# Kernel optimization log

Measured on AMD Instinct MI355X. Metric: run time of the kernel, lower is better.

## Reference

```python
import jax, jax.numpy as jnp
import numpy as np

# Graph layout: B equal-sized graphs, contiguous node ids.
B, NG, EG = 64, 2000, 64000          # graphs, nodes/graph, edges/graph
K = 1600                              # ceil(0.8 * NG) — TopKPooling ratio=0.8
N, E = B * NG, B * EG
FEAT_DIM, EMB, G1, G2, DENSE, NCLS = 10000, 64, 32, 32, 64, 10


def setup_inputs() -> dict:
    key = jax.random.key(0)
    ks = jax.random.split(key, 12)
    x = jax.random.randint(ks[0], (N, 1), 0, FEAT_DIM)
    # random edges within each graph, then offset by graph base node id
    e = jax.random.randint(ks[1], (2, B, EG), 0, NG) + (jnp.arange(B) * NG)[None, :, None]
    edge_index = e.reshape(2, E)
    batch = jnp.repeat(jnp.arange(B), NG)
    sc = 0.05
    return {
        "x": x, "edge_index": edge_index, "batch": batch,
        "emb": jax.random.normal(ks[2], (FEAT_DIM, EMB), jnp.float32) * sc,
        "W1": jax.random.normal(ks[3], (EMB, G1), jnp.float32) * sc,
        "b1": jnp.zeros((G1,), jnp.float32),
        "W2": jax.random.normal(ks[4], (G1, G2), jnp.float32) * sc,
        "b2": jnp.zeros((G2,), jnp.float32),
        "pool_w": jax.random.normal(ks[5], (G2,), jnp.float32) * sc,
        "dense_W": jax.random.normal(ks[6], (G2, DENSE), jnp.float32) * sc,
        "dense_b": jnp.zeros((DENSE,), jnp.float32),
        "out_W": jax.random.normal(ks[7], (DENSE, NCLS), jnp.float32) * sc,
        "out_b": jnp.zeros((NCLS,), jnp.float32),
    }


def gcn_layer(h, src, dst, W, b):
    """PyG GCNConv: add self-loops, symmetric D^-1/2 A D^-1/2 aggregation."""
    n = h.shape[0]
    loop = jnp.arange(n)
    s = jnp.concatenate([src, loop])
    d = jnp.concatenate([dst, loop])
    h = h @ W                                                   # [N, out]
    deg = jax.ops.segment_sum(jnp.ones_like(d, dtype=h.dtype), d, num_segments=n)
    dinv = jnp.where(deg > 0, deg ** -0.5, 0.0)
    norm = dinv[s] * dinv[d]                                    # [E+N]
    out = jax.ops.segment_sum(h[s] * norm[:, None], d, num_segments=n)
    return out + b


def reference(x, edge_index, batch, emb, W1, b1, W2, b2, pool_w,
              dense_W, dense_b, out_W, out_b):
    h = emb[x[:, 0]]                                            # [N, EMB]
    src, dst = edge_index[0], edge_index[1]
    h = jax.nn.relu(gcn_layer(h, src, dst, W1, b1))
    h = jax.nn.relu(gcn_layer(h, src, dst, W2, b2))
    # TopKPooling: score = tanh(x.w / ||w||); keep top ceil(0.8*NG) per graph,
    # scale kept features by their scores. Equal graph sizes -> static shapes.
    score = jnp.tanh(h @ pool_w / jnp.linalg.norm(pool_w))      # [N]
    sb = score.reshape(B, NG)
    hb = h.reshape(B, NG, G2)
    vals, idx = jax.lax.top_k(sb, K)                            # [B, K]
    hp = jnp.take_along_axis(hb, idx[:, :, None], axis=1) * vals[:, :, None]
    g = hp.max(axis=1)                                          # global max pool [B, G2]
    d = jax.nn.relu(g @ dense_W + dense_b)
    return d @ out_W + out_b                                    # [B, NCLS]
```

## Files before the change

### kernel.cpp

```cpp
#include <hip/hip_runtime.h>
#include <hip/hip_fp16.h>
#include <math.h>

#define NB 64
#define NGRAPH 2000
#define EGRAPH 64000
#define NN (NB*NGRAPH)
#define NE (NB*EGRAPH)
#define KSEL 1600
#define FEAT 10000
#define EMBD 64
#define G1D 32
#define G2D 32
#define DENSED 64
#define NCLSD 10
#define NCHUNK 8
#define CHUNK_E (EGRAPH/NCHUNK)
#define NQD 8
#define QNODES (NGRAPH/NQD)
#define LOUT_CAP 10000


__device__ __forceinline__ float4 ld_row8h(const char* base, unsigned byteoff)
{
    uint2 u = *(const uint2*)(base + byteoff);
    __half2 p0 = *(__half2*)&u.x;
    __half2 p1 = *(__half2*)&u.y;
    float2 f0 = __half22float2(p0);
    float2 f1 = __half22float2(p1);
    return make_float4(f0.x, f0.y, f1.x, f1.y);
}

__device__ __forceinline__ void st_row8h(__half* dst, float4 v)
{
    __half2 p0 = __floats2half2_rn(v.x, v.y);
    __half2 p1 = __floats2half2_rn(v.z, v.w);
    uint2 u;
    u.x = *(unsigned*)&p0;
    u.y = *(unsigned*)&p1;
    *(uint2*)dst = u;
}

__global__ __launch_bounds__(256) void prep_kernel(const int* __restrict__ ei,
                                                   int* __restrict__ chist,
                                                   const float* __restrict__ emb,
                                                   const float* __restrict__ W1,
                                                   float* __restrict__ embW)
{
    __shared__ float shmem[2048];
    const int tid = threadIdx.x;
    if (blockIdx.x < 512) {
        int* hist = (int*)shmem;
        const int lb = blockIdx.x;
        const int xcd = lb & 7, t = lb >> 3;
        const int g = xcd * 8 + (t >> 3);
        const int q = t & 7;
        const int base_e = g * EGRAPH + q * CHUNK_E;
        const int base_n = g * NGRAPH;
        for (int v = tid; v < NGRAPH; v += 256) hist[v] = 0;
        __syncthreads();
        for (int k = tid; k < CHUNK_E; k += 256) {
            int d = ei[NE + base_e + k];
            atomicAdd(&hist[d - base_n], 1);
        }
        __syncthreads();
        int* out = chist + (size_t)(g * NCHUNK + q) * NGRAPH;
        for (int v = tid; v < NGRAPH; v += 256) out[v] = hist[v];
    } else {
        float* W1s = shmem;
        for (int i = tid; i < EMBD * G1D; i += 256) W1s[i] = W1[i];
        __syncthreads();
        int id = (blockIdx.x - 512) * 256 + tid;
        int r = id >> 5, c = id & 31;
        if (r >= FEAT) return;
        const float* er = emb + r * EMBD;
        float acc = 0.f;
        #pragma unroll 8
        for (int k = 0; k < EMBD; ++k) acc += er[k] * W1s[k * G1D + c];
        embW[r * G1D + c] = acc;
    }
}

__global__ __launch_bounds__(256) void scan_graph(const int* __restrict__ chist,
                                                  float* __restrict__ dinv,
                                                  int* __restrict__ row_start)
{
    __shared__ int hist[NGRAPH];
    __shared__ int csA[256];
    __shared__ int csB[256];
    const int b = (blockIdx.x & 7) * 8 + (blockIdx.x >> 3);
    const int tid = threadIdx.x;
    const int base_n = b * NGRAPH, base_e = b * EGRAPH;
    const int* ch = chist + (size_t)b * NCHUNK * NGRAPH;

    for (int v = tid; v < NGRAPH; v += 256) {
        int tot = 0;
        #pragma unroll
        for (int q = 0; q < NCHUNK; ++q) tot += ch[q * NGRAPH + v];
        hist[v] = tot;
        dinv[base_n + v] = rsqrtf((float)(tot + 1));
    }
    __syncthreads();
    if (tid < 250) {
        int s = 0;
        #pragma unroll
        for (int i = 0; i < 8; ++i) s += hist[tid * 8 + i];
        csA[tid] = s;
    }
    __syncthreads();
    int* sb = csA; int* db = csB;
    for (int off = 1; off < 256; off <<= 1) {
        int v = 0;
        if (tid < 250) { v = sb[tid]; if (tid >= off) v += sb[tid - off]; }
        if (tid < 250) db[tid] = v;
        __syncthreads();
        int* t = sb; sb = db; db = t;
    }
    if (tid < 250) {
        int run = (tid == 0) ? 0 : sb[tid - 1];
        #pragma unroll
        for (int i = 0; i < 8; ++i) {
            int idx = tid * 8 + i;
            int c = hist[idx];
            row_start[base_n + idx] = base_e + run;
            run += c;
        }
    }
}

__global__ __launch_bounds__(1024) void mid_kernel(const int* __restrict__ ei,
                                                   const int* __restrict__ row_start,
                                                   int* __restrict__ csr,
                                                   const int* __restrict__ x,
                                                   const float* __restrict__ embW,
                                                   const float* __restrict__ dinv,
                                                   __half* __restrict__ A)
{
    __shared__ int cur[QNODES];
    __shared__ int lout[LOUT_CAP];
    const int tid = threadIdx.x;
    if (blockIdx.x < 512) {
        const int lb = blockIdx.x;
        const int xcd = lb & 7, t = lb >> 3;
        const int g = xcd * 8 + (t >> 3);
        const int qd = t & 7;
        const int base_n = g * NGRAPH;
        const int lo = qd * QNODES;
        const int base = row_start[base_n + lo];
        const int qend = (g == NB - 1 && qd == NQD - 1) ? NE
                         : row_start[base_n + lo + QNODES];
        for (int v = tid; v < QNODES; v += 1024)
            cur[v] = row_start[base_n + lo + v] - base;
        __syncthreads();
        const int4* srcp = (const int4*)(ei + g * EGRAPH);
        const int4* dstp = (const int4*)(ei + NE + g * EGRAPH);
        const int sub = base_n + lo;
        for (int k = tid; k < EGRAPH / 4; k += 1024) {
            int4 d4 = dstp[k];
            int4 s4 = srcp[k];
            int d, pos;
            d = d4.x - sub;
            if ((unsigned)d < (unsigned)QNODES) {
                pos = atomicAdd(&cur[d], 1);
                if (pos < LOUT_CAP) lout[pos] = s4.x << 6;
            }
            d = d4.y - sub;
            if ((unsigned)d < (unsigned)QNODES) {
                pos = atomicAdd(&cur[d], 1);
                if (pos < LOUT_CAP) lout[pos] = s4.y << 6;
            }
            d = d4.z - sub;
            if ((unsigned)d < (unsigned)QNODES) {
                pos = atomicAdd(&cur[d], 1);
                if (pos < LOUT_CAP) lout[pos] = s4.z << 6;
            }
            d = d4.w - sub;
            if ((unsigned)d < (unsigned)QNODES) {
                pos = atomicAdd(&cur[d], 1);
                if (pos < LOUT_CAP) lout[pos] = s4.w << 6;
            }
        }
        __syncthreads();
        int size = qend - base;
        if (size > LOUT_CAP) size = LOUT_CAP;
        for (int i = tid; i < size; i += 1024)
            csr[base + i] = lout[i];
    } else {
        int id = (blockIdx.x - 512) * 1024 + tid;
        int v = id >> 3, r = id & 7;
        int xv = x[v];
        float dv = dinv[v];
        float4 e = ((const float4*)(embW + (size_t)xv * G1D))[r];
        e.x *= dv; e.y *= dv; e.z *= dv; e.w *= dv;
        st_row8h(A + (size_t)v * G1D + r * 4, e);
    }
}


__global__ __launch_bounds__(256) void agg1_kernel(const __half* __restrict__ Ain,
                                                   const float* __restrict__ dinv,
                                                   const int* __restrict__ row_start,
                                                   const int* __restrict__ csr,
                                                   const float* __restrict__ b1,
                                                   const float* __restrict__ W2,
                                                   __half* __restrict__ Bout)
{
    __shared__ float hsh[8][G2D];
    const int lb = blockIdx.x;
    const int xcd = lb & 7, idx = lb >> 3;
    const int b = xcd * 8 + (idx >> 5);
    const int blk = idx & 31;
    const int half_id = threadIdx.x >> 5;
    const int hl = threadIdx.x & 31;
    const int slot = hl >> 3;
    const int r = hl & 7;
    const int roff = r << 3;
    const char* Abase = (const char*)Ain;
    const int base_n = b * NGRAPH;
    const float4 bias4 = ((const float4*)b1)[r];

    float w2c[G1D];
    #pragma unroll
    for (int k = 0; k < G1D; ++k) w2c[k] = W2[k * G2D + hl];

    const int vloc0 = blk * 64 + half_id * 8;
    int v = base_n + ((vloc0 < NGRAPH) ? vloc0 : NGRAPH - 1);
    int rs = row_start[v];
    int re = (v == NN - 1) ? NE : row_start[v + 1];
    int s0 = csr[rs + slot];
    int s1 = csr[rs + slot + 4];
    int s2 = csr[rs + slot + 8];
    int s3 = csr[rs + slot + 12];

    for (int i = 0; i < 8; ++i) {
        int vloc = vloc0 + i;
        if (vloc >= NGRAPH) break;
        int re_next = (v + 1 >= NN - 1) ? NE : row_start[v + 2];
        int n0 = csr[re + slot];
        int n1 = csr[re + slot + 4];
        int n2 = csr[re + slot + 8];
        int n3 = csr[re + slot + 12];

        int me = rs + ((re - rs) & ~15);
        float4 acc0 = make_float4(0.f, 0.f, 0.f, 0.f);
        float4 acc1 = make_float4(0.f, 0.f, 0.f, 0.f);
        float4 acc2 = make_float4(0.f, 0.f, 0.f, 0.f);
        float4 acc3 = make_float4(0.f, 0.f, 0.f, 0.f);
        if (slot == 0)
            acc0 = ld_row8h(Abase, (unsigned)(v * (G1D * 2) + roff));
        int j = rs + slot;
        while (j < me) {
            int jn = j + 16;
            int t0 = csr[jn];
            int t1 = csr[jn + 4];
            int t2 = csr[jn + 8];
            int t3 = csr[jn + 12];
            float4 a0 = ld_row8h(Abase, (unsigned)(s0 + roff));
            float4 a1 = ld_row8h(Abase, (unsigned)(s1 + roff));
            float4 a2 = ld_row8h(Abase, (unsigned)(s2 + roff));
            float4 a3 = ld_row8h(Abase, (unsigned)(s3 + roff));
            acc0.x += a0.x; acc0.y += a0.y; acc0.z += a0.z; acc0.w += a0.w;
            acc1.x += a1.x; acc1.y += a1.y; acc1.z += a1.z; acc1.w += a1.w;
            acc2.x += a2.x; acc2.y += a2.y; acc2.z += a2.z; acc2.w += a2.w;
            acc3.x += a3.x; acc3.y += a3.y; acc3.z += a3.z; acc3.w += a3.w;
            j = jn; s0 = t0; s1 = t1; s2 = t2; s3 = t3;
        }
        {
            int jt = me + slot;
            if (jt < re) {
                float4 a = ld_row8h(Abase, (unsigned)(s0 + roff));
                acc0.x += a.x; acc0.y += a.y; acc0.z += a.z; acc0.w += a.w;
            }
            if (jt + 4 < re) {
                float4 a = ld_row8h(Abase, (unsigned)(s1 + roff));
                acc1.x += a.x; acc1.y += a.y; acc1.z += a.z; acc1.w += a.w;
            }
            if (jt + 8 < re) {
                float4 a = ld_row8h(Abase, (unsigned)(s2 + roff));
                acc2.x += a.x; acc2.y += a.y; acc2.z += a.z; acc2.w += a.w;
            }
            if (jt + 12 < re) {
                float4 a = ld_row8h(Abase, (unsigned)(s3 + roff));
                acc3.x += a.x; acc3.y += a.y; acc3.z += a.z; acc3.w += a.w;
            }
        }
        float4 acc;
        acc.x = (acc0.x + acc1.x) + (acc2.x + acc3.x);
        acc.y = (acc0.y + acc1.y) + (acc2.y + acc3.y);
        acc.z = (acc0.z + acc1.z) + (acc2.z + acc3.z);
        acc.w = (acc0.w + acc1.w) + (acc2.w + acc3.w);
        #pragma unroll
        for (int off = 8; off <= 16; off <<= 1) {
            acc.x += __shfl_xor(acc.x, off, 32);
            acc.y += __shfl_xor(acc.y, off, 32);
            acc.z += __shfl_xor(acc.z, off, 32);
            acc.w += __shfl_xor(acc.w, off, 32);
        }
        float dv = dinv[v];
        if (slot == 0) {
            float4 h4;
            h4.x = fmaxf(dv * acc.x + bias4.x, 0.f);
            h4.y = fmaxf(dv * acc.y + bias4.y, 0.f);
            h4.z = fmaxf(dv * acc.z + bias4.z, 0.f);
            h4.w = fmaxf(dv * acc.w + bias4.w, 0.f);
            ((float4*)&hsh[half_id][0])[r] = h4;
        }
        float o0 = 0.f, o1 = 0.f, o2 = 0.f, o3 = 0.f;
        const float4* hrow = (const float4*)&hsh[half_id][0];
        #pragma unroll
        for (int q = 0; q < 8; ++q) {
            float4 hh = hrow[q];
            o0 += hh.x * w2c[4 * q + 0];
            o1 += hh.y * w2c[4 * q + 1];
            o2 += hh.z * w2c[4 * q + 2];
            o3 += hh.w * w2c[4 * q + 3];
        }
        Bout[(size_t)v * G2D + hl] = __float2half(dv * ((o0 + o1) + (o2 + o3)));
        v = v + 1;
        rs = re; re = re_next; s0 = n0; s1 = n1; s2 = n2; s3 = n3;
    }
}

__global__ __launch_bounds__(256) void agg2_kernel(const __half* __restrict__ Bin,
                                                   const float* __restrict__ dinv,
                                                   const int* __restrict__ row_start,
                                                   const int* __restrict__ csr,
                                                   const float* __restrict__ b2,
                                                   const float* __restrict__ pool_w,
                                                   __half* __restrict__ h2out,
                                                   float* __restrict__ scores)
{
    const int lb = blockIdx.x;
    const int xcd = lb & 7, idx = lb >> 3;
    const int b = xcd * 8 + (idx >> 5);
    const int blk = idx & 31;
    const int half_id = threadIdx.x >> 5;
    const int hl = threadIdx.x & 31;
    const int slot = hl >> 3;
    const int r = hl & 7;
    const int roff = r << 3;
    const char* Bbase = (const char*)Bin;
    const int base_n = b * NGRAPH;
    const float4 bias4 = ((const float4*)b2)[r];
    const float4 pw4 = ((const float4*)pool_w)[r];

    float pw = pool_w[hl];
    float nsq = pw * pw;
    #pragma unroll
    for (int off = 16; off; off >>= 1) nsq += __shfl_xor(nsq, off, 32);
    const float inv_norm = rsqrtf(nsq);

    const int vloc0 = blk * 64 + half_id * 8;
    int v = base_n + ((vloc0 < NGRAPH) ? vloc0 : NGRAPH - 1);
    int rs = row_start[v];
    int re = (v == NN - 1) ? NE : row_start[v + 1];
    int s0 = csr[rs + slot];
    int s1 = csr[rs + slot + 4];
    int s2 = csr[rs + slot + 8];
    int s3 = csr[rs + slot + 12];

    for (int i = 0; i < 8; ++i) {
        int vloc = vloc0 + i;
        if (vloc >= NGRAPH) break;
        int re_next = (v + 1 >= NN - 1) ? NE : row_start[v + 2];
        int n0 = csr[re + slot];
        int n1 = csr[re + slot + 4];
        int n2 = csr[re + slot + 8];
        int n3 = csr[re + slot + 12];

        int me = rs + ((re - rs) & ~15);
        float4 acc0 = make_float4(0.f, 0.f, 0.f, 0.f);
        float4 acc1 = make_float4(0.f, 0.f, 0.f, 0.f);
        float4 acc2 = make_float4(0.f, 0.f, 0.f, 0.f);
        float4 acc3 = make_float4(0.f, 0.f, 0.f, 0.f);
        if (slot == 0)
            acc0 = ld_row8h(Bbase, (unsigned)(v * (G2D * 2) + roff));
        int j = rs + slot;
        while (j < me) {
            int jn = j + 16;
            int t0 = csr[jn];
            int t1 = csr[jn + 4];
            int t2 = csr[jn + 8];
            int t3 = csr[jn + 12];
            float4 a0 = ld_row8h(Bbase, (unsigned)(s0 + roff));
            float4 a1 = ld_row8h(Bbase, (unsigned)(s1 + roff));
            float4 a2 = ld_row8h(Bbase, (unsigned)(s2 + roff));
            float4 a3 = ld_row8h(Bbase, (unsigned)(s3 + roff));
            acc0.x += a0.x; acc0.y += a0.y; acc0.z += a0.z; acc0.w += a0.w;
            acc1.x += a1.x; acc1.y += a1.y; acc1.z += a1.z; acc1.w += a1.w;
            acc2.x += a2.x; acc2.y += a2.y; acc2.z += a2.z; acc2.w += a2.w;
            acc3.x += a3.x; acc3.y += a3.y; acc3.z += a3.z; acc3.w += a3.w;
            j = jn; s0 = t0; s1 = t1; s2 = t2; s3 = t3;
        }
        {
            int jt = me + slot;
            if (jt < re) {
                float4 a = ld_row8h(Bbase, (unsigned)(s0 + roff));
                acc0.x += a.x; acc0.y += a.y; acc0.z += a.z; acc0.w += a.w;
            }
            if (jt + 4 < re) {
                float4 a = ld_row8h(Bbase, (unsigned)(s1 + roff));
                acc1.x += a.x; acc1.y += a.y; acc1.z += a.z; acc1.w += a.w;
            }
            if (jt + 8 < re) {
                float4 a = ld_row8h(Bbase, (unsigned)(s2 + roff));
                acc2.x += a.x; acc2.y += a.y; acc2.z += a.z; acc2.w += a.w;
            }
            if (jt + 12 < re) {
                float4 a = ld_row8h(Bbase, (unsigned)(s3 + roff));
                acc3.x += a.x; acc3.y += a.y; acc3.z += a.z; acc3.w += a.w;
            }
        }
        float4 acc;
        acc.x = (acc0.x + acc1.x) + (acc2.x + acc3.x);
        acc.y = (acc0.y + acc1.y) + (acc2.y + acc3.y);
        acc.z = (acc0.z + acc1.z) + (acc2.z + acc3.z);
        acc.w = (acc0.w + acc1.w) + (acc2.w + acc3.w);
        #pragma unroll
        for (int off = 8; off <= 16; off <<= 1) {
            acc.x += __shfl_xor(acc.x, off, 32);
            acc.y += __shfl_xor(acc.y, off, 32);
            acc.z += __shfl_xor(acc.z, off, 32);
            acc.w += __shfl_xor(acc.w, off, 32);
        }
        float dv = dinv[v];
        float4 h4;
        h4.x = fmaxf(dv * acc.x + bias4.x, 0.f);
        h4.y = fmaxf(dv * acc.y + bias4.y, 0.f);
        h4.z = fmaxf(dv * acc.z + bias4.z, 0.f);
        h4.w = fmaxf(dv * acc.w + bias4.w, 0.f);
        if (slot == 0)
            st_row8h(h2out + (size_t)v * G2D + r * 4, h4);
        float t = h4.x * pw4.x + h4.y * pw4.y + h4.z * pw4.z + h4.w * pw4.w;
        t += __shfl_xor(t, 1, 32);
        t += __shfl_xor(t, 2, 32);
        t += __shfl_xor(t, 4, 32);
        if (hl == 0) scores[v] = tanhf(t * inv_norm);
        v = v + 1;
        rs = re; re = re_next; s0 = n0; s1 = n1; s2 = n2; s3 = n3;
    }
}

__global__ __launch_bounds__(256) void topk_pool_mlp(const __half* __restrict__ h2,
                                                     const float* __restrict__ scores,
                                                     const float* __restrict__ dense_W,
                                                     const float* __restrict__ dense_b,
                                                     const float* __restrict__ out_W,
                                                     const float* __restrict__ out_b,
                                                     float* __restrict__ out)
{
    __shared__ unsigned keys[NGRAPH];
    __shared__ float    sval[NGRAPH];
    __shared__ unsigned char inc[NGRAPH];
    __shared__ int  hist[256];
    __shared__ int  csA[256];
    __shared__ int  csB[256];
    __shared__ int  sel[2];
    __shared__ int  redc[4];
    __shared__ float redf[32][32];
    __shared__ float gvec[32];
    __shared__ float dvec[DENSED];
    const int b = (blockIdx.x & 7) * 8 + (blockIdx.x >> 3);
    const int tid = threadIdx.x;
    const int base_n = b * NGRAPH;

    for (int v = tid; v < NGRAPH; v += 256) {
        float f = scores[base_n + v];
        sval[v] = f;
        unsigned u = __float_as_uint(f);
        keys[v] = (u & 0x80000000u) ? ~u : (u | 0x80000000u);
    }
    __syncthreads();

    unsigned T = 0;
    int need = KSEL;
    #pragma unroll
    for (int pass = 0; pass < 4; ++pass) {
        const int s = 24 - pass * 8;
        const unsigned hi_mask = (pass == 0) ? 0u : (0xFFFFFFFFu << (s + 8));
        hist[tid] = 0;
        __syncthreads();
        for (int v = tid; v < NGRAPH; v += 256) {
            unsigned k = keys[v];
            if ((k & hi_mask) == (T & hi_mask))
                atomicAdd(&hist[(k >> s) & 255], 1);
        }
        __syncthreads();
        csA[tid] = hist[255 - tid];
        __syncthreads();
        int* sb = csA; int* db = csB;
        for (int off = 1; off < 256; off <<= 1) {
            int val = sb[tid];
            if (tid >= off) val += sb[tid - off];
            db[tid] = val;
            __syncthreads();
            int* t = sb; sb = db; db = t;
        }
        {
            const int d = tid;
            int suf_d = sb[255 - d];
            int suf_d1 = (d == 255) ? 0 : sb[254 - d];
            if (suf_d >= need && suf_d1 < need) {
                sel[0] = d;
                sel[1] = suf_d1;
            }
        }
        __syncthreads();
        T |= ((unsigned)sel[0]) << s;
        need -= sel[1];
        __syncthreads();
    }

    const int wid = tid >> 6, ln = tid & 63;
    int cg = 0, ce = 0;
    for (int v = tid; v < NGRAPH; v += 256) {
        cg += (keys[v] > T) ? 1 : 0;
        ce += (keys[v] == T) ? 1 : 0;
    }
    int packed = (cg << 16) | ce;
    #pragma unroll
    for (int off = 32; off; off >>= 1) packed += __shfl_down(packed, off, 64);
    if (ln == 0) redc[wid] = packed;
    __syncthreads();
    int tot = redc[0] + redc[1] + redc[2] + redc[3];
    int m_gt = tot >> 16, m_eq = tot & 0xffff;
    int needed = KSEL - m_gt;
    float fT = (T & 0x80000000u) ? __uint_as_float(T & 0x7fffffffu)
                                 : __uint_as_float(~T);
    if (m_eq == needed || fT == 0.0f) {
        for (int v = tid; v < NGRAPH; v += 256) inc[v] = (keys[v] >= T) ? 1 : 0;
    } else {
        if (tid == 0) {
            int take = 0;
            for (int v = 0; v < NGRAPH; ++v) {
                unsigned k = keys[v];
                if (k > T) inc[v] = 1;
                else if (k == T && take < needed) { inc[v] = 1; ++take; }
                else inc[v] = 0;
            }
        }
    }
    __syncthreads();

    {
        const int rowslot = tid >> 3;
        const int c4 = tid & 7;
        float4 m4 = make_float4(-INFINITY, -INFINITY, -INFINITY, -INFINITY);
        const char* h2base = (const char*)h2;
        for (int v = rowslot; v < NGRAPH; v += 32) {
            float4 hrow = ld_row8h(h2base,
                                   (unsigned)((base_n + v) * (G2D * 2) + c4 * 8));
            float sv = inc[v] ? sval[v] : 0.f;
            float big = inc[v] ? 0.f : -INFINITY;
            m4.x = fmaxf(m4.x, sv * hrow.x + big);
            m4.y = fmaxf(m4.y, sv * hrow.y + big);
            m4.z = fmaxf(m4.z, sv * hrow.z + big);
            m4.w = fmaxf(m4.w, sv * hrow.w + big);
        }
        redf[rowslot][c4 * 4 + 0] = m4.x;
        redf[rowslot][c4 * 4 + 1] = m4.y;
        redf[rowslot][c4 * 4 + 2] = m4.z;
        redf[rowslot][c4 * 4 + 3] = m4.w;
    }
    __syncthreads();
    if (tid < 32) {
        float g = redf[0][tid];
        #pragma unroll
        for (int rr = 1; rr < 32; ++rr) g = fmaxf(g, redf[rr][tid]);
        gvec[tid] = g;
    }
    __syncthreads();
    if (tid < DENSED) {
        float t = dense_b[tid];
        #pragma unroll
        for (int k = 0; k < G2D; ++k) t += gvec[k] * dense_W[k * DENSED + tid];
        dvec[tid] = fmaxf(t, 0.f);
    }
    __syncthreads();
    if (tid < NCLSD) {
        float o = out_b[tid];
        #pragma unroll
        for (int j = 0; j < DENSED; ++j) o += dvec[j] * out_W[j * NCLSD + tid];
        out[b * NCLSD + tid] = o;
    }
}

extern "C" void kernel_launch(void* const* d_in, const int* in_sizes, int n_in,
                              void* d_out, int out_size, void* d_ws, size_t ws_size,
                              hipStream_t stream)
{
    (void)in_sizes; (void)n_in; (void)out_size; (void)ws_size;
    const int*   x       = (const int*)  d_in[0];
    const int*   edge    = (const int*)  d_in[1];
    const float* emb     = (const float*)d_in[3];
    const float* W1      = (const float*)d_in[4];
    const float* b1      = (const float*)d_in[5];
    const float* W2      = (const float*)d_in[6];
    const float* b2      = (const float*)d_in[7];
    const float* pool_w  = (const float*)d_in[8];
    const float* dense_W = (const float*)d_in[9];
    const float* dense_b = (const float*)d_in[10];
    const float* out_W   = (const float*)d_in[11];
    const float* out_b   = (const float*)d_in[12];
    float* outp = (float*)d_out;

    char* ws = (char*)d_ws;
    float*  embW      = (float*)ws;
    __half* Ah        = (__half*)(ws + 1280000);
    __half* Bh        = (__half*)(ws + 1280000 + 8192000);
    float*  dinv      = (float*)(ws + 1280000 + 2*8192000);
    int*    row_start = (int*)((char*)dinv + (size_t)NN*4);
    int*    csr       = (int*)((char*)row_start + (size_t)NN*4);
    float*  scores    = (float*)((char*)csr + (size_t)(NE+16)*4);

    int* chist = (int*)Bh;

    prep_kernel<<<512 + (FEAT * G1D) / 256, 256, 0, stream>>>(edge, chist, emb, W1, embW);
    scan_graph<<<NB, 256, 0, stream>>>(chist, dinv, row_start);
    mid_kernel<<<512 + (NN * 8) / 1024, 1024, 0, stream>>>(edge, row_start, csr,
                                                           x, embW, dinv, Ah);
    agg1_kernel<<<NB * 32, 256, 0, stream>>>(Ah, dinv, row_start, csr, b1, W2, Bh);
    agg2_kernel<<<NB * 32, 256, 0, stream>>>(Bh, dinv, row_start, csr, b2, pool_w, Ah, scores);
    topk_pool_mlp<<<NB, 256, 0, stream>>>(Ah, scores, dense_W, dense_b, out_W, out_b, outp);
}
```

Measured before the change: 249.7 us.

## Stage per-graph feature table in LDS for both aggregation kernels

Each aggregation block now covers a quarter of one graph with 1024 threads and first copies that graph's 2000x32 half-precision feature table (128 KB) into shared memory. Neighbour gathers then read from LDS through graph-local offsets instead of issuing scattered global loads. This removes repeated random global/L2 traffic, but the grid shrinks to 256 blocks. The large LDS footprint limits each CU to one block, and every block pays a full-table preload even though it only serves a quarter of the nodes.

```diff
diff --git a/kernel.cpp b/kernel.cpp
--- a/kernel.cpp
+++ b/kernel.cpp
@@ -19,6 +19,8 @@
 #define NQD 8
 #define QNODES (NGRAPH/NQD)
 #define LOUT_CAP 10000
+#define AGG_PARTS 4
+#define NPP (NGRAPH/AGG_PARTS)
 
 
 __device__ __forceinline__ float4 ld_row8h(const char* base, unsigned byteoff)
@@ -197,49 +199,60 @@
 }
 
 
-__global__ __launch_bounds__(256) void agg1_kernel(const __half* __restrict__ Ain,
-                                                   const float* __restrict__ dinv,
-                                                   const int* __restrict__ row_start,
-                                                   const int* __restrict__ csr,
-                                                   const float* __restrict__ b1,
-                                                   const float* __restrict__ W2,
-                                                   __half* __restrict__ Bout)
-{
-    __shared__ float hsh[8][G2D];
+__global__ __launch_bounds__(1024) void agg1_kernel(const __half* __restrict__ Ain,
+                                                    const float* __restrict__ dinv,
+                                                    const int* __restrict__ row_start,
+                                                    const int* __restrict__ csr,
+                                                    const float* __restrict__ b1,
+                                                    const float* __restrict__ W2,
+                                                    __half* __restrict__ Bout)
+{
+    __shared__ uint4 table4[NGRAPH * 4];
+    __shared__ float hsh[32][G2D];
     const int lb = blockIdx.x;
-    const int xcd = lb & 7, idx = lb >> 3;
-    const int b = xcd * 8 + (idx >> 5);
-    const int blk = idx & 31;
-    const int half_id = threadIdx.x >> 5;
-    const int hl = threadIdx.x & 31;
+    const int xcd = lb & 7, t = lb >> 3;
+    const int b = xcd * 8 + (t >> 2);
+    const int part = t & 3;
+    const int tid = threadIdx.x;
+    const int base_n = b * NGRAPH;
+    const int boff = base_n << 6;
+
+    {
+        const uint4* src = (const uint4*)(Ain + (size_t)base_n * G1D);
+        for (int i = tid; i < NGRAPH * 4; i += 1024) table4[i] = src[i];
+    }
+    __syncthreads();
+
+    const char* Lbase = (const char*)table4;
+    const int hw = tid >> 5;
+    const int hl = tid & 31;
     const int slot = hl >> 3;
     const int r = hl & 7;
     const int roff = r << 3;
-    const char* Abase = (const char*)Ain;
-    const int base_n = b * NGRAPH;
     const float4 bias4 = ((const float4*)b1)[r];
 
     float w2c[G1D];
     #pragma unroll
     for (int k = 0; k < G1D; ++k) w2c[k] = W2[k * G2D + hl];
 
-    const int vloc0 = blk * 64 + half_id * 8;
-    int v = base_n + ((vloc0 < NGRAPH) ? vloc0 : NGRAPH - 1);
+    const int vloc0 = part * NPP + hw * 16;
+    const int vend = part * NPP + NPP;
+    int v = base_n + vloc0;
     int rs = row_start[v];
     int re = (v == NN - 1) ? NE : row_start[v + 1];
-    int s0 = csr[rs + slot];
-    int s1 = csr[rs + slot + 4];
-    int s2 = csr[rs + slot + 8];
-    int s3 = csr[rs + slot + 12];
-
-    for (int i = 0; i < 8; ++i) {
+    int s0 = csr[rs + slot] - boff;
+    int s1 = csr[rs + slot + 4] - boff;
+    int s2 = csr[rs + slot + 8] - boff;
+    int s3 = csr[rs + slot + 12] - boff;
+
+    for (int i = 0; i < 16; ++i) {
         int vloc = vloc0 + i;
-        if (vloc >= NGRAPH) break;
+        if (vloc >= vend) break;
         int re_next = (v + 1 >= NN - 1) ? NE : row_start[v + 2];
-        int n0 = csr[re + slot];
-        int n1 = csr[re + slot + 4];
-        int n2 = csr[re + slot + 8];
-        int n3 = csr[re + slot + 12];
+        int n0 = csr[re + slot] - boff;
+        int n1 = csr[re + slot + 4] - boff;
+        int n2 = csr[re + slot + 8] - boff;
+        int n3 = csr[re + slot + 12] - boff;
 
         int me = rs + ((re - rs) & ~15);
         float4 acc0 = make_float4(0.f, 0.f, 0.f, 0.f);
@@ -247,18 +260,18 @@
         float4 acc2 = make_float4(0.f, 0.f, 0.f, 0.f);
         float4 acc3 = make_float4(0.f, 0.f, 0.f, 0.f);
         if (slot == 0)
-            acc0 = ld_row8h(Abase, (unsigned)(v * (G1D * 2) + roff));
+            acc0 = ld_row8h(Lbase, (unsigned)((vloc << 6) + roff));
         int j = rs + slot;
         while (j < me) {
             int jn = j + 16;
-            int t0 = csr[jn];
-            int t1 = csr[jn + 4];
-            int t2 = csr[jn + 8];
-            int t3 = csr[jn + 12];
-            float4 a0 = ld_row8h(Abase, (unsigned)(s0 + roff));
-            float4 a1 = ld_row8h(Abase, (unsigned)(s1 + roff));
-            float4 a2 = ld_row8h(Abase, (unsigned)(s2 + roff));
-            float4 a3 = ld_row8h(Abase, (unsigned)(s3 + roff));
+            int t0 = csr[jn] - boff;
+            int t1 = csr[jn + 4] - boff;
+            int t2 = csr[jn + 8] - boff;
+            int t3 = csr[jn + 12] - boff;
+            float4 a0 = ld_row8h(Lbase, (unsigned)(s0 + roff));
+            float4 a1 = ld_row8h(Lbase, (unsigned)(s1 + roff));
+            float4 a2 = ld_row8h(Lbase, (unsigned)(s2 + roff));
+            float4 a3 = ld_row8h(Lbase, (unsigned)(s3 + roff));
             acc0.x += a0.x; acc0.y += a0.y; acc0.z += a0.z; acc0.w += a0.w;
             acc1.x += a1.x; acc1.y += a1.y; acc1.z += a1.z; acc1.w += a1.w;
             acc2.x += a2.x; acc2.y += a2.y; acc2.z += a2.z; acc2.w += a2.w;
@@ -268,19 +281,19 @@
         {
             int jt = me + slot;
             if (jt < re) {
-                float4 a = ld_row8h(Abase, (unsigned)(s0 + roff));
+                float4 a = ld_row8h(Lbase, (unsigned)(s0 + roff));
                 acc0.x += a.x; acc0.y += a.y; acc0.z += a.z; acc0.w += a.w;
             }
             if (jt + 4 < re) {
-                float4 a = ld_row8h(Abase, (unsigned)(s1 + roff));
+                float4 a = ld_row8h(Lbase, (unsigned)(s1 + roff));
                 acc1.x += a.x; acc1.y += a.y; acc1.z += a.z; acc1.w += a.w;
             }
             if (jt + 8 < re) {
-                float4 a = ld_row8h(Abase, (unsigned)(s2 + roff));
+                float4 a = ld_row8h(Lbase, (unsigned)(s2 + roff));
                 acc2.x += a.x; acc2.y += a.y; acc2.z += a.z; acc2.w += a.w;
             }
             if (jt + 12 < re) {
-                float4 a = ld_row8h(Abase, (unsigned)(s3 + roff));
+                float4 a = ld_row8h(Lbase, (unsigned)(s3 + roff));
                 acc3.x += a.x; acc3.y += a.y; acc3.z += a.z; acc3.w += a.w;
             }
         }
@@ -303,10 +316,10 @@
             h4.y = fmaxf(dv * acc.y + bias4.y, 0.f);
             h4.z = fmaxf(dv * acc.z + bias4.z, 0.f);
             h4.w = fmaxf(dv * acc.w + bias4.w, 0.f);
-            ((float4*)&hsh[half_id][0])[r] = h4;
+            ((float4*)&hsh[hw][0])[r] = h4;
         }
         float o0 = 0.f, o1 = 0.f, o2 = 0.f, o3 = 0.f;
-        const float4* hrow = (const float4*)&hsh[half_id][0];
+        const float4* hrow = (const float4*)&hsh[hw][0];
         #pragma unroll
         for (int q = 0; q < 8; ++q) {
             float4 hh = hrow[q];
@@ -321,26 +334,36 @@
     }
 }
 
-__global__ __launch_bounds__(256) void agg2_kernel(const __half* __restrict__ Bin,
-                                                   const float* __restrict__ dinv,
-                                                   const int* __restrict__ row_start,
-                                                   const int* __restrict__ csr,
-                                                   const float* __restrict__ b2,
-                                                   const float* __restrict__ pool_w,
-                                                   __half* __restrict__ h2out,
-                                                   float* __restrict__ scores)
-{
+__global__ __launch_bounds__(1024) void agg2_kernel(const __half* __restrict__ Bin,
+                                                    const float* __restrict__ dinv,
+                                                    const int* __restrict__ row_start,
+                                                    const int* __restrict__ csr,
+                                                    const float* __restrict__ b2,
+                                                    const float* __restrict__ pool_w,
+                                                    __half* __restrict__ h2out,
+                                                    float* __restrict__ scores)
+{
+    __shared__ uint4 table4[NGRAPH * 4];
     const int lb = blockIdx.x;
-    const int xcd = lb & 7, idx = lb >> 3;
-    const int b = xcd * 8 + (idx >> 5);
-    const int blk = idx & 31;
-    const int half_id = threadIdx.x >> 5;
-    const int hl = threadIdx.x & 31;
+    const int xcd = lb & 7, t = lb >> 3;
+    const int b = xcd * 8 + (t >> 2);
+    const int part = t & 3;
+    const int tid = threadIdx.x;
+    const int base_n = b * NGRAPH;
+    const int boff = base_n << 6;
+
+    {
+        const uint4* src = (const uint4*)(Bin + (size_t)base_n * G1D);
+        for (int i = tid; i < NGRAPH * 4; i += 1024) table4[i] = src[i];
+    }
+    __syncthreads();
+
+    const char* Lbase = (const char*)table4;
+    const int hw = tid >> 5;
+    const int hl = tid & 31;
     const int slot = hl >> 3;
     const int r = hl & 7;
     const int roff = r << 3;
-    const char* Bbase = (const char*)Bin;
-    const int base_n = b * NGRAPH;
     const float4 bias4 = ((const float4*)b2)[r];
     const float4 pw4 = ((const float4*)pool_w)[r];
 
@@ -350,23 +373,24 @@
     for (int off = 16; off; off >>= 1) nsq += __shfl_xor(nsq, off, 32);
     const float inv_norm = rsqrtf(nsq);
 
-    const int vloc0 = blk * 64 + half_id * 8;
-    int v = base_n + ((vloc0 < NGRAPH) ? vloc0 : NGRAPH - 1);
+    const int vloc0 = part * NPP + hw * 16;
+    const int vend = part * NPP + NPP;
+    int v = base_n + vloc0;
     int rs = row_start[v];
     int re = (v == NN - 1) ? NE : row_start[v + 1];
-    int s0 = csr[rs + slot];
-    int s1 = csr[rs + slot + 4];
-    int s2 = csr[rs + slot + 8];
-    int s3 = csr[rs + slot + 12];
-
-    for (int i = 0; i < 8; ++i) {
+    int s0 = csr[rs + slot] - boff;
+    int s1 = csr[rs + slot + 4] - boff;
+    int s2 = csr[rs + slot + 8] - boff;
+    int s3 = csr[rs + slot + 12] - boff;
+
+    for (int i = 0; i < 16; ++i) {
         int vloc = vloc0 + i;
-        if (vloc >= NGRAPH) break;
+        if (vloc >= vend) break;
         int re_next = (v + 1 >= NN - 1) ? NE : row_start[v + 2];
-        int n0 = csr[re + slot];
-        int n1 = csr[re + slot + 4];
-        int n2 = csr[re + slot + 8];
-        int n3 = csr[re + slot + 12];
+        int n0 = csr[re + slot] - boff;
+        int n1 = csr[re + slot + 4] - boff;
+        int n2 = csr[re + slot + 8] - boff;
+        int n3 = csr[re + slot + 12] - boff;
 
         int me = rs + ((re - rs) & ~15);
         float4 acc0 = make_float4(0.f, 0.f, 0.f, 0.f);
@@ -374,18 +398,18 @@
         float4 acc2 = make_float4(0.f, 0.f, 0.f, 0.f);
         float4 acc3 = make_float4(0.f, 0.f, 0.f, 0.f);
         if (slot == 0)
-            acc0 = ld_row8h(Bbase, (unsigned)(v * (G2D * 2) + roff));
+            acc0 = ld_row8h(Lbase, (unsigned)((vloc << 6) + roff));
         int j = rs + slot;
         while (j < me) {
             int jn = j + 16;
-            int t0 = csr[jn];
-            int t1 = csr[jn + 4];
-            int t2 = csr[jn + 8];
-            int t3 = csr[jn + 12];
-            float4 a0 = ld_row8h(Bbase, (unsigned)(s0 + roff));
-            float4 a1 = ld_row8h(Bbase, (unsigned)(s1 + roff));
-            float4 a2 = ld_row8h(Bbase, (unsigned)(s2 + roff));
-            float4 a3 = ld_row8h(Bbase, (unsigned)(s3 + roff));
+            int t0 = csr[jn] - boff;
+            int t1 = csr[jn + 4] - boff;
+            int t2 = csr[jn + 8] - boff;
+            int t3 = csr[jn + 12] - boff;
+            float4 a0 = ld_row8h(Lbase, (unsigned)(s0 + roff));
+            float4 a1 = ld_row8h(Lbase, (unsigned)(s1 + roff));
+            float4 a2 = ld_row8h(Lbase, (unsigned)(s2 + roff));
+            float4 a3 = ld_row8h(Lbase, (unsigned)(s3 + roff));
             acc0.x += a0.x; acc0.y += a0.y; acc0.z += a0.z; acc0.w += a0.w;
             acc1.x += a1.x; acc1.y += a1.y; acc1.z += a1.z; acc1.w += a1.w;
             acc2.x += a2.x; acc2.y += a2.y; acc2.z += a2.z; acc2.w += a2.w;
@@ -395,19 +419,19 @@
         {
             int jt = me + slot;
             if (jt < re) {
-                float4 a = ld_row8h(Bbase, (unsigned)(s0 + roff));
+                float4 a = ld_row8h(Lbase, (unsigned)(s0 + roff));
                 acc0.x += a.x; acc0.y += a.y; acc0.z += a.z; acc0.w += a.w;
             }
             if (jt + 4 < re) {
-                float4 a = ld_row8h(Bbase, (unsigned)(s1 + roff));
+                float4 a = ld_row8h(Lbase, (unsigned)(s1 + roff));
                 acc1.x += a.x; acc1.y += a.y; acc1.z += a.z; acc1.w += a.w;
             }
             if (jt + 8 < re) {
-                float4 a = ld_row8h(Bbase, (unsigned)(s2 + roff));
+                float4 a = ld_row8h(Lbase, (unsigned)(s2 + roff));
                 acc2.x += a.x; acc2.y += a.y; acc2.z += a.z; acc2.w += a.w;
             }
             if (jt + 12 < re) {
-                float4 a = ld_row8h(Bbase, (unsigned)(s3 + roff));
+                float4 a = ld_row8h(Lbase, (unsigned)(s3 + roff));
                 acc3.x += a.x; acc3.y += a.y; acc3.z += a.z; acc3.w += a.w;
             }
         }
@@ -431,11 +455,11 @@
         h4.w = fmaxf(dv * acc.w + bias4.w, 0.f);
         if (slot == 0)
             st_row8h(h2out + (size_t)v * G2D + r * 4, h4);
-        float t = h4.x * pw4.x + h4.y * pw4.y + h4.z * pw4.z + h4.w * pw4.w;
-        t += __shfl_xor(t, 1, 32);
-        t += __shfl_xor(t, 2, 32);
-        t += __shfl_xor(t, 4, 32);
-        if (hl == 0) scores[v] = tanhf(t * inv_norm);
+        float tt = h4.x * pw4.x + h4.y * pw4.y + h4.z * pw4.z + h4.w * pw4.w;
+        tt += __shfl_xor(tt, 1, 32);
+        tt += __shfl_xor(tt, 2, 32);
+        tt += __shfl_xor(tt, 4, 32);
+        if (hl == 0) scores[v] = tanhf(tt * inv_norm);
         v = v + 1;
         rs = re; re = re_next; s0 = n0; s1 = n1; s2 = n2; s3 = n3;
     }
@@ -619,7 +643,7 @@
     scan_graph<<<NB, 256, 0, stream>>>(chist, dinv, row_start);
     mid_kernel<<<512 + (NN * 8) / 1024, 1024, 0, stream>>>(edge, row_start, csr,
                                                            x, embW, dinv, Ah);
-    agg1_kernel<<<NB * 32, 256, 0, stream>>>(Ah, dinv, row_start, csr, b1, W2, Bh);
-    agg2_kernel<<<NB * 32, 256, 0, stream>>>(Bh, dinv, row_start, csr, b2, pool_w, Ah, scores);
+    agg1_kernel<<<NB * AGG_PARTS, 1024, 0, stream>>>(Ah, dinv, row_start, csr, b1, W2, Bh);
+    agg2_kernel<<<NB * AGG_PARTS, 1024, 0, stream>>>(Bh, dinv, row_start, csr, b2, pool_w, Ah, scores);
     topk_pool_mlp<<<NB, 256, 0, stream>>>(Ah, scores, dense_W, dense_b, out_W, out_b, outp);
 }
```

Result: faster. 226.0 us (-9.5%).
